# Kernel tuning notes

Measured on AMD Instinct MI355X. Metric: run time of the kernel, lower is better.

## Reference

```python
import jax, jax.numpy as jnp
import numpy as np

N_NODES = 10240
N_EDGES = 40960
N_GRAPHS = 256
F_XD = 78
SEQ = 1000
VOCAB = 26
EMB = 128
NEG_SLOPE = 0.2


def gat_conv(x, src, dst, W, att_src, att_dst, bias, heads, f_out):
    """PyG GATConv (concat=True, self-loops, leaky_relu 0.2, dst-segment softmax)."""
    N = x.shape[0]
    h = (x @ W).reshape(N, heads, f_out)                      # [N,H,F]
    a_s = jnp.sum(h * att_src[None], axis=-1)                 # [N,H]
    a_d = jnp.sum(h * att_dst[None], axis=-1)                 # [N,H]
    loop = jnp.arange(N, dtype=src.dtype)
    s = jnp.concatenate([src, loop])                          # add self-loops
    d = jnp.concatenate([dst, loop])
    e = jax.nn.leaky_relu(a_s[s] + a_d[d], NEG_SLOPE)         # [E',H]
    m = jax.ops.segment_max(e, d, num_segments=N)             # stable softmax per dst
    e = jnp.exp(e - m[d])
    denom = jax.ops.segment_sum(e, d, num_segments=N)
    alpha = e / (denom[d] + 1e-16)                            # [E',H]
    out = jax.ops.segment_sum(alpha[:, :, None] * h[s], d, num_segments=N)
    return out.reshape(N, heads * f_out) + bias


def conv1d(x, w, b):
    y = jax.lax.conv_general_dilated(x, w, window_strides=(1,), padding='VALID',
                                     dimension_numbers=('NCH', 'OIH', 'NCH'))
    return y + b[None, :, None]


def maxpool1d(x, k):
    return jax.lax.reduce_window(x, -jnp.inf, jax.lax.max, (1, 1, k), (1, 1, k), 'VALID')


def setup_inputs() -> dict:
    key = jax.random.key(0)
    ks = jax.random.split(key, 32)
    x = jax.random.normal(ks[0], (N_NODES, F_XD), jnp.float32)
    src = jax.random.randint(ks[1], (N_EDGES,), 0, N_NODES, dtype=jnp.int32)
    dst = jax.random.randint(ks[2], (N_EDGES,), 0, N_NODES, dtype=jnp.int32)
    dst = jnp.where(dst == src, (dst + 1) % N_NODES, dst)     # no pre-existing self loops
    edge_index = jnp.stack([src, dst])
    batch = jnp.repeat(jnp.arange(N_GRAPHS, dtype=jnp.int32), N_NODES // N_GRAPHS)
    target = jax.random.randint(ks[3], (N_GRAPHS, SEQ), 0, VOCAB, dtype=jnp.int32)
    def w(k, shape):
        return jax.random.normal(k, shape, jnp.float32) * 0.05
    p = {
        'W1': w(ks[4], (78, 10 * 78)), 'as1': w(ks[5], (10, 78)), 'ad1': w(ks[6], (10, 78)), 'b1': jnp.zeros((780,), jnp.float32),
        'W2': w(ks[7], (780, 2 * 780)), 'as2': w(ks[8], (2, 780)), 'ad2': w(ks[9], (2, 780)), 'b2': jnp.zeros((1560,), jnp.float32),
        'W3': w(ks[10], (1560, 3120)), 'as3': w(ks[11], (1, 3120)), 'ad3': w(ks[12], (1, 3120)), 'b3': jnp.zeros((3120,), jnp.float32),
        'fc_g1_w': w(ks[13], (3120, 1024)), 'fc_g1_b': jnp.zeros((1024,), jnp.float32),
        'fc_g2_w': w(ks[14], (1024, 128)), 'fc_g2_b': jnp.zeros((128,), jnp.float32),
        'emb_xt': w(ks[15], (VOCAB, EMB)),
        'cw1': w(ks[16], (32, 1000, 8)), 'cb1': jnp.zeros((32,), jnp.float32),
        'cw2': w(ks[17], (64, 32, 8)), 'cb2': jnp.zeros((64,), jnp.float32),
        'cw3': w(ks[18], (96, 64, 8)), 'cb3': jnp.zeros((96,), jnp.float32),
        'cw4': w(ks[19], (128, 96, 8)), 'cb4': jnp.zeros((128,), jnp.float32),
        'fc1_xt_w': w(ks[20], (128 * 33, 1024)), 'fc1_xt_b': jnp.zeros((1024,), jnp.float32),
        'fc2_xt_w': w(ks[21], (1024, 128)), 'fc2_xt_b': jnp.zeros((128,), jnp.float32),
        'fc1_w': w(ks[22], (256, 1024)), 'fc1_b': jnp.zeros((1024,), jnp.float32),
        'fc2_w': w(ks[23], (1024, 256)), 'fc2_b': jnp.zeros((256,), jnp.float32),
        'out_w': w(ks[24], (256, 1)), 'out_b': jnp.zeros((1,), jnp.float32),
    }
    return {'x': x, 'edge_index': edge_index, 'batch': batch, 'target': target, **p}


def reference(x, edge_index, batch, target,
              W1, as1, ad1, b1, W2, as2, ad2, b2, W3, as3, ad3, b3,
              fc_g1_w, fc_g1_b, fc_g2_w, fc_g2_b, emb_xt,
              cw1, cb1, cw2, cb2, cw3, cb3, cw4, cb4,
              fc1_xt_w, fc1_xt_b, fc2_xt_w, fc2_xt_b,
              fc1_w, fc1_b, fc2_w, fc2_b, out_w, out_b):
    src, dst = edge_index[0], edge_index[1]
    # --- GAT branch (dropout layers are identity in eval mode) ---
    h = jax.nn.elu(gat_conv(x, src, dst, W1, as1, ad1, b1, 10, 78))
    h = jax.nn.relu(gat_conv(h, src, dst, W2, as2, ad2, b2, 2, 780))
    h = jax.nn.relu(gat_conv(h, src, dst, W3, as3, ad3, b3, 1, 3120))
    g = jax.ops.segment_max(h, batch, num_segments=N_GRAPHS)   # global max pool
    g = jax.nn.relu(g @ fc_g1_w + fc_g1_b)
    g = g @ fc_g2_w + fc_g2_b                                  # [B,128]
    # --- protein CNN branch ---
    e = emb_xt[target]                                         # [B,1000,128]
    c = jax.nn.relu(conv1d(e, cw1, cb1))                       # [B,32,121]
    c = jax.nn.relu(conv1d(c, cw2, cb2))                       # [B,64,114]
    c = jax.nn.relu(conv1d(c, cw3, cb3))                       # [B,96,107]
    c = jax.nn.relu(conv1d(c, cw4, cb4))                       # [B,128,100]
    c = maxpool1d(c, 3)                                        # [B,128,33]
    xt = c.reshape(N_GRAPHS, 128 * 33)
    xt = jax.nn.relu(xt @ fc1_xt_w + fc1_xt_b)
    xt = xt @ fc2_xt_w + fc2_xt_b                              # [B,128]
    # --- fusion head ---
    xc = jnp.concatenate([g, xt], axis=1)                      # [B,256]
    xc = jax.nn.relu(xc @ fc1_w + fc1_b)
    xc = jax.nn.relu(xc @ fc2_w + fc2_b)
    return xc @ out_w + out_b                                  # [B,1]
```

## Files before the change

### kernel.cpp

```cpp
#include <hip/hip_runtime.h>
#include <hip/hip_bf16.h>
#include <math.h>

static const int NNODES = 10240;
static const int NEDGES = 40960;
static const int NB     = 256;
static const int VOCAB  = 26;
static const int EMB    = 128;
static const int LP     = 128;
static const int C1SPLIT = 8;

typedef short bf16x8 __attribute__((ext_vector_type(8)));
typedef float f32x4  __attribute__((ext_vector_type(4)));

__device__ __forceinline__ float bf16bits2float(short s) {
    return __uint_as_float(((unsigned)(unsigned short)s) << 16);
}

__global__ __launch_bounds__(256) void gemm_f32_splitk_sl(
    const float* __restrict__ A, const float* __restrict__ B,
    float* __restrict__ P, int M, int N, int K, int kchunk)
{
    __shared__ float As[16][65];
    __shared__ float Bs[16][65];
    int tid = threadIdx.x;
    int bm = blockIdx.y * 64;
    int bn = blockIdx.x * 64;
    int z = blockIdx.z;
    int k0 = z * kchunk;
    int k1 = min(k0 + kchunk, K);
    int tx = tid & 15, ty = tid >> 4;
    float acc[4][4] = {};
    for (int kb = k0; kb < k1; kb += 16) {
#pragma unroll
        for (int l = 0; l < 4; ++l) {
            int idx = tid + l * 256;
            int r = idx >> 4, c = idx & 15;
            int gr = bm + r, gc = kb + c;
            As[c][r] = (gr < M && gc < k1) ? A[(size_t)gr * K + gc] : 0.f;
        }
#pragma unroll
        for (int l = 0; l < 4; ++l) {
            int idx = tid + l * 256;
            int r = idx >> 6, c = idx & 63;
            int gr = kb + r, gc = bn + c;
            Bs[r][c] = (gr < k1 && gc < N) ? B[(size_t)gr * N + gc] : 0.f;
        }
        __syncthreads();
#pragma unroll
        for (int kk = 0; kk < 16; ++kk) {
            float a[4], b[4];
#pragma unroll
            for (int i = 0; i < 4; ++i) a[i] = As[kk][ty * 4 + i];
#pragma unroll
            for (int j = 0; j < 4; ++j) b[j] = Bs[kk][tx * 4 + j];
#pragma unroll
            for (int i = 0; i < 4; ++i)
#pragma unroll
                for (int j = 0; j < 4; ++j)
                    acc[i][j] += a[i] * b[j];
        }
        __syncthreads();
    }
    float* Pz = P + (size_t)z * M * N;
#pragma unroll
    for (int i = 0; i < 4; ++i) {
        int gr = bm + ty * 4 + i;
        if (gr >= M) continue;
#pragma unroll
        for (int j = 0; j < 4; ++j) {
            int gc = bn + tx * 4 + j;
            if (gc >= N) continue;
            Pz[(size_t)gr * N + gc] = acc[i][j];
        }
    }
}

template<int ACT>
__global__ void reduce_bias_act_ld_kernel(const float* __restrict__ P,
                                          const float* __restrict__ bias,
                                          float* __restrict__ C,
                                          int M, int N, int S, int ldC)
{
    int t = blockIdx.x * 256 + threadIdx.x;
    if (t >= M * N) return;
    int r = t / N, c = t - r * N;
    float v = bias[c];
    for (int s = 0; s < S; ++s) v += P[(size_t)s * M * N + t];
    if (ACT == 1) v = fmaxf(v, 0.f);
    C[(size_t)r * ldC + c] = v;
}

__global__ void out_head_kernel(const float* __restrict__ f2,
                                const float* __restrict__ w,
                                const float* __restrict__ b,
                                float* __restrict__ out)
{
    __shared__ float sw[256];
    int t = threadIdx.x;
    sw[t] = w[t];
    __syncthreads();
    float acc = 0.f;
    const float* row = f2 + (size_t)t * 256;
    for (int k = 0; k < 256; ++k) acc += row[k] * sw[k];
    out[t] = acc + b[0];
}

__global__ void cast_a_kernel(const float* __restrict__ in, __hip_bfloat16* __restrict__ out,
                              int M, int K, int Kp)
{
    int idx = blockIdx.x * 256 + threadIdx.x;
    if (idx >= M * Kp) return;
    int r = idx / Kp, k = idx - r * Kp;
    out[idx] = __float2bfloat16(k < K ? in[(size_t)r * K + k] : 0.f);
}

__global__ __launch_bounds__(256) void transpose_cast_kernel(
    const float* __restrict__ in, __hip_bfloat16* __restrict__ out,
    int K, int N, int Kp, int Npad)
{
    __shared__ float tile[32][33];
    int k0 = blockIdx.x * 32;
    int n0 = blockIdx.y * 32;
    int tx = threadIdx.x & 31;
    int ty = threadIdx.x >> 5;
#pragma unroll
    for (int j = 0; j < 4; ++j) {
        int k = k0 + ty + j * 8, n = n0 + tx;
        tile[ty + j * 8][tx] = (k < K && n < N) ? in[(size_t)k * N + n] : 0.f;
    }
    __syncthreads();
#pragma unroll
    for (int j = 0; j < 4; ++j) {
        int n = n0 + ty + j * 8, k = k0 + tx;
        if (n < Npad && k < Kp)
            out[(size_t)n * Kp + k] = __float2bfloat16(tile[tx][ty + j * 8]);
    }
}

__global__ void conv_wt_all_kernel(
    const float* __restrict__ cw2, const float* __restrict__ cw3,
    const float* __restrict__ cw4, const float* __restrict__ cw1,
    __hip_bfloat16* __restrict__ wt2, __hip_bfloat16* __restrict__ wt3,
    __hip_bfloat16* __restrict__ wt4, float* __restrict__ wt1f)
{
    int idx = blockIdx.x * 256 + threadIdx.x;
    const int n2 = 64 * 32 * 8, n3 = 96 * 64 * 8, n4 = 128 * 96 * 8;
    if (idx < n2) {
        int o = idx / (32 * 8), rem = idx - o * 32 * 8;
        int i = rem >> 3, k = rem & 7;
        wt2[(size_t)o * 256 + k * 32 + i] = __float2bfloat16(cw2[idx]);
    } else if (idx < n2 + n3) {
        int j = idx - n2;
        int o = j / (64 * 8), rem = j - o * 64 * 8;
        int i = rem >> 3, k = rem & 7;
        wt3[(size_t)o * 512 + k * 64 + i] = __float2bfloat16(cw3[j]);
    } else if (idx < n2 + n3 + n4) {
        int j = idx - n2 - n3;
        int o = j / (96 * 8), rem = j - o * 96 * 8;
        int i = rem >> 3, k = rem & 7;
        wt4[(size_t)o * 768 + k * 96 + i] = __float2bfloat16(cw4[j]);
    } else {
        int j = idx - n2 - n3 - n4;
        if (j >= 32 * 8000) return;
        int o = j / 8000, rem = j - o * 8000;
        int i = rem >> 3, k = rem & 7;
        wt1f[(size_t)i * 256 + o * 8 + k] = cw1[j];
    }
}

__device__ __forceinline__ void stage_tile(
    const __hip_bfloat16* __restrict__ gA, int ldA,
    const __hip_bfloat16* __restrict__ gB, int ldB,
    short* ldsbuf, int w, int l)
{
#pragma unroll
    for (int j = 0; j < 4; ++j) {
        int u = (w * 4 + j) * 64 + l;
        int r = u >> 3, s = u & 7;
        const __hip_bfloat16* src = gA + (size_t)r * ldA + ((s ^ (r & 7)) << 3);
        __builtin_amdgcn_global_load_lds(
            (const __attribute__((address_space(1))) void*)src,
            (__attribute__((address_space(3))) void*)(ldsbuf + (w * 4 + j) * 512),
            16, 0, 0);
    }
#pragma unroll
    for (int j = 0; j < 4; ++j) {
        int u = (w * 4 + j) * 64 + l;
        int r = u >> 3, s = u & 7;
        const __hip_bfloat16* src = gB + (size_t)r * ldB + ((s ^ (r & 7)) << 3);
        __builtin_amdgcn_global_load_lds(
            (const __attribute__((address_space(1))) void*)src,
            (__attribute__((address_space(3))) void*)(ldsbuf + 8192 + (w * 4 + j) * 512),
            16, 0, 0);
    }
}

__global__ __launch_bounds__(256, 2) void gemm_mfma_bf16(
    const __hip_bfloat16* __restrict__ A,
    const __hip_bfloat16* __restrict__ Bt,
    __hip_bfloat16* __restrict__ C, int M, int N, int Kp, int ldC)
{
    __shared__ __align__(16) short lds[2][16384];
    const int tid = threadIdx.x;
    const int w = tid >> 6, l = tid & 63;

    int nwg = gridDim.x * gridDim.y;
    int wg = blockIdx.y * gridDim.x + blockIdx.x;
    int q = nwg >> 3, r8 = nwg & 7;
    int xcd = wg & 7, lo = wg >> 3;
    int swz = (xcd < r8) ? (xcd * (q + 1) + lo) : (r8 * (q + 1) + (xcd - r8) * q + lo);
    const int bm = (swz / gridDim.x) * 128, bn = (swz % gridDim.x) * 128;

    const int wr = w >> 1, wc = w & 1;
    const int lane15 = l & 15, lhi = l >> 4;

    const __hip_bfloat16* gA = A + (size_t)bm * Kp;
    const __hip_bfloat16* gB = Bt + (size_t)bn * Kp;

    f32x4 acc[4][4] = {};

    const int nk = Kp >> 6;
    stage_tile(gA, Kp, gB, Kp, &lds[0][0], w, l);
    __syncthreads();
    int cur = 0;
    for (int t = 0; t < nk; ++t) {
        if (t + 1 < nk)
            stage_tile(gA + (t + 1) * 64, Kp, gB + (t + 1) * 64, Kp, &lds[cur ^ 1][0], w, l);
        const short* bA = &lds[cur][0];
        const short* bB = &lds[cur][8192];
#pragma unroll
        for (int ks = 0; ks < 2; ++ks) {
            bf16x8 af[4], bfr[4];
#pragma unroll
            for (int m = 0; m < 4; ++m) {
                int r = wr * 64 + m * 16 + lane15;
                int slot = (ks * 4 + lhi) ^ (r & 7);
                af[m] = *(const bf16x8*)(bA + r * 64 + slot * 8);
            }
#pragma unroll
            for (int n = 0; n < 4; ++n) {
                int r = wc * 64 + n * 16 + lane15;
                int slot = (ks * 4 + lhi) ^ (r & 7);
                bfr[n] = *(const bf16x8*)(bB + r * 64 + slot * 8);
            }
#pragma unroll
            for (int m = 0; m < 4; ++m)
#pragma unroll
                for (int n = 0; n < 4; ++n)
                    acc[m][n] = __builtin_amdgcn_mfma_f32_16x16x32_bf16(
                        af[m], bfr[n], acc[m][n], 0, 0, 0);
        }
        __syncthreads();
        cur ^= 1;
    }
#pragma unroll
    for (int m = 0; m < 4; ++m) {
#pragma unroll
        for (int n = 0; n < 4; ++n) {
            int col = bn + wc * 64 + n * 16 + lane15;
            if (col >= N) continue;
            int row0 = bm + wr * 64 + m * 16 + lhi * 4;
#pragma unroll
            for (int q2 = 0; q2 < 4; ++q2)
                C[(size_t)(row0 + q2) * ldC + col] = __float2bfloat16(acc[m][n][q2]);
        }
    }
}

__global__ __launch_bounds__(256, 2) void gemm_mfma_splitk(
    const __hip_bfloat16* __restrict__ A,
    const __hip_bfloat16* __restrict__ Bt,
    float* __restrict__ P, int M, int N, int Kp, int tps)
{
    __shared__ __align__(16) short lds[2][16384];
    const int tid = threadIdx.x;
    const int w = tid >> 6, l = tid & 63;
    const int bm = blockIdx.y * 128, bn = blockIdx.x * 128;
    const int z = blockIdx.z;
    const int wr = w >> 1, wc = w & 1;
    const int lane15 = l & 15, lhi = l >> 4;

    const __hip_bfloat16* gA = A + (size_t)bm * Kp + z * tps * 64;
    const __hip_bfloat16* gB = Bt + (size_t)bn * Kp + z * tps * 64;

    f32x4 acc[4][4] = {};

    const int nk = tps;
    stage_tile(gA, Kp, gB, Kp, &lds[0][0], w, l);
    __syncthreads();
    int cur = 0;
    for (int t = 0; t < nk; ++t) {
        if (t + 1 < nk)
            stage_tile(gA + (t + 1) * 64, Kp, gB + (t + 1) * 64, Kp, &lds[cur ^ 1][0], w, l);
        const short* bA = &lds[cur][0];
        const short* bB = &lds[cur][8192];
#pragma unroll
        for (int ks = 0; ks < 2; ++ks) {
            bf16x8 af[4], bfr[4];
#pragma unroll
            for (int m = 0; m < 4; ++m) {
                int r = wr * 64 + m * 16 + lane15;
                int slot = (ks * 4 + lhi) ^ (r & 7);
                af[m] = *(const bf16x8*)(bA + r * 64 + slot * 8);
            }
#pragma unroll
            for (int n = 0; n < 4; ++n) {
                int r = wc * 64 + n * 16 + lane15;
                int slot = (ks * 4 + lhi) ^ (r & 7);
                bfr[n] = *(const bf16x8*)(bB + r * 64 + slot * 8);
            }
#pragma unroll
            for (int m = 0; m < 4; ++m)
#pragma unroll
                for (int n = 0; n < 4; ++n)
                    acc[m][n] = __builtin_amdgcn_mfma_f32_16x16x32_bf16(
                        af[m], bfr[n], acc[m][n], 0, 0, 0);
        }
        __syncthreads();
        cur ^= 1;
    }
    float* Pz = P + (size_t)z * M * N;
#pragma unroll
    for (int m = 0; m < 4; ++m) {
#pragma unroll
        for (int n = 0; n < 4; ++n) {
            int col = bn + wc * 64 + n * 16 + lane15;
            if (col >= N) continue;
            int row0 = bm + wr * 64 + m * 16 + lhi * 4;
#pragma unroll
            for (int q2 = 0; q2 < 4; ++q2) {
                int row = row0 + q2;
                if (row < M) Pz[(size_t)row * N + col] = acc[m][n][q2];
            }
        }
    }
}

template<int Ci, int Co, int Lout>
__global__ __launch_bounds__(256, 2) void gemm_conv_bf16(
    const __hip_bfloat16* __restrict__ A,
    const __hip_bfloat16* __restrict__ Bt,
    const float* __restrict__ bias,
    __hip_bfloat16* __restrict__ C)
{
    const int Kp = 8 * Ci;
    __shared__ __align__(16) short lds[2][16384];
    const int tid = threadIdx.x;
    const int w = tid >> 6, l = tid & 63;
    const int bm = blockIdx.y * 128;
    const int wr = w >> 1, wc = w & 1;
    const int lane15 = l & 15, lhi = l >> 4;

    const __hip_bfloat16* gA = A + (size_t)bm * Ci;
    const __hip_bfloat16* gB = Bt;

    f32x4 acc[4][4] = {};

    const int nk = Kp >> 6;
    stage_tile(gA, Ci, gB, Kp, &lds[0][0], w, l);
    __syncthreads();
    int cur = 0;
    for (int t = 0; t < nk; ++t) {
        if (t + 1 < nk)
            stage_tile(gA + (t + 1) * 64, Ci, gB + (t + 1) * 64, Kp, &lds[cur ^ 1][0], w, l);
        const short* bA = &lds[cur][0];
        const short* bB = &lds[cur][8192];
#pragma unroll
        for (int ks = 0; ks < 2; ++ks) {
            bf16x8 af[4], bfr[4];
#pragma unroll
            for (int m = 0; m < 4; ++m) {
                int r = wr * 64 + m * 16 + lane15;
                int slot = (ks * 4 + lhi) ^ (r & 7);
                af[m] = *(const bf16x8*)(bA + r * 64 + slot * 8);
            }
#pragma unroll
            for (int n = 0; n < 4; ++n) {
                int r = wc * 64 + n * 16 + lane15;
                int slot = (ks * 4 + lhi) ^ (r & 7);
                bfr[n] = *(const bf16x8*)(bB + r * 64 + slot * 8);
            }
#pragma unroll
            for (int m = 0; m < 4; ++m)
#pragma unroll
                for (int n = 0; n < 4; ++n)
                    acc[m][n] = __builtin_amdgcn_mfma_f32_16x16x32_bf16(
                        af[m], bfr[n], acc[m][n], 0, 0, 0);
        }
        __syncthreads();
        cur ^= 1;
    }
#pragma unroll
    for (int m = 0; m < 4; ++m) {
#pragma unroll
        for (int n = 0; n < 4; ++n) {
            int col = wc * 64 + n * 16 + lane15;
            if (col >= Co) continue;
            float bb = bias[col];
            int lr0 = wr * 64 + m * 16 + lhi * 4;
#pragma unroll
            for (int q2 = 0; q2 < 4; ++q2) {
                int lr = lr0 + q2;
                if (lr < Lout)
                    C[((size_t)bm + lr) * Co + col] =
                        __float2bfloat16(fmaxf(acc[m][n][q2] + bb, 0.f));
            }
        }
    }
}

__global__ __launch_bounds__(256, 2) void gemm_conv4_pool_bf16(
    const __hip_bfloat16* __restrict__ A,
    const __hip_bfloat16* __restrict__ Bt,
    const float* __restrict__ bias,
    __hip_bfloat16* __restrict__ xtb)
{
    const int Ci = 96, Kp = 768;
    __shared__ __align__(16) short lds[2][16384];
    const int tid = threadIdx.x;
    const int w = tid >> 6, l = tid & 63;
    const int bm = blockIdx.y * 128;
    const int wr = w >> 1, wc = w & 1;
    const int lane15 = l & 15, lhi = l >> 4;

    const __hip_bfloat16* gA = A + (size_t)bm * Ci;
    const __hip_bfloat16* gB = Bt;

    f32x4 acc[4][4] = {};

    const int nk = Kp >> 6;
    stage_tile(gA, Ci, gB, Kp, &lds[0][0], w, l);
    __syncthreads();
    int cur = 0;
    for (int t = 0; t < nk; ++t) {
        if (t + 1 < nk)
            stage_tile(gA + (t + 1) * 64, Ci, gB + (t + 1) * 64, Kp, &lds[cur ^ 1][0], w, l);
        const short* bA = &lds[cur][0];
        const short* bB = &lds[cur][8192];
#pragma unroll
        for (int ks = 0; ks < 2; ++ks) {
            bf16x8 af[4], bfr[4];
#pragma unroll
            for (int m = 0; m < 4; ++m) {
                int r = wr * 64 + m * 16 + lane15;
                int slot = (ks * 4 + lhi) ^ (r & 7);
                af[m] = *(const bf16x8*)(bA + r * 64 + slot * 8);
            }
#pragma unroll
            for (int n = 0; n < 4; ++n) {
                int r = wc * 64 + n * 16 + lane15;
                int slot = (ks * 4 + lhi) ^ (r & 7);
                bfr[n] = *(const bf16x8*)(bB + r * 64 + slot * 8);
            }
#pragma unroll
            for (int m = 0; m < 4; ++m)
#pragma unroll
                for (int n = 0; n < 4; ++n)
                    acc[m][n] = __builtin_amdgcn_mfma_f32_16x16x32_bf16(
                        af[m], bfr[n], acc[m][n], 0, 0, 0);
        }
        __syncthreads();
        cur ^= 1;
    }
    float* pbuf = (float*)&lds[0][0];
#pragma unroll
    for (int m = 0; m < 4; ++m) {
#pragma unroll
        for (int n = 0; n < 4; ++n) {
            int col = wc * 64 + n * 16 + lane15;
            float bb = bias[col];
            int lr0 = wr * 64 + m * 16 + lhi * 4;
#pragma unroll
            for (int q2 = 0; q2 < 4; ++q2)
                pbuf[(lr0 + q2) * 128 + col] = acc[m][n][q2] + bb;
        }
    }
    __syncthreads();
    int nb = blockIdx.y;
    for (int idx = tid; idx < 4352; idx += 256) {
        __hip_bfloat16 v;
        if (idx >= 4224) {
            v = __float2bfloat16(0.f);
        } else {
            int c = idx / 33, tp = idx - c * 33;
            float m3 = fmaxf(fmaxf(pbuf[(tp * 3) * 128 + c], pbuf[(tp * 3 + 1) * 128 + c]),
                             pbuf[(tp * 3 + 2) * 128 + c]);
            v = __float2bfloat16(fmaxf(m3, 0.f));
        }
        xtb[(size_t)nb * 4352 + idx] = v;
    }
}

__global__ void attn_ab_kernel(const __hip_bfloat16* __restrict__ lin, int Ftp,
                               const float* __restrict__ att_s,
                               const float* __restrict__ att_d,
                               float* __restrict__ a_s, float* __restrict__ a_d,
                               int H, int F)
{
    int bid = blockIdx.x;
    int n = bid / H, h = bid - n * H;
    int lane = threadIdx.x;
    const __hip_bfloat16* row = lin + (size_t)n * Ftp + h * F;
    const float* wsrc = att_s + h * F;
    const float* wdst = att_d + h * F;
    float ss = 0.f, sd = 0.f;
    for (int f = lane; f < F; f += 64) {
        float v = __bfloat162float(row[f]);
        ss += v * wsrc[f];
        sd += v * wdst[f];
    }
    for (int o = 32; o; o >>= 1) {
        ss += __shfl_down(ss, o);
        sd += __shfl_down(sd, o);
    }
    if (lane == 0) { a_s[bid] = ss; a_d[bid] = sd; }
}

__global__ void deg_kernel(const int* __restrict__ ei, int* __restrict__ deg,
                           int E, int Etot)
{
    int e = blockIdx.x * 256 + threadIdx.x;
    if (e >= Etot) return;
    int d = (e < E) ? ei[E + e] : e - E;
    atomicAdd(&deg[d], 1);
}

__global__ __launch_bounds__(256) void scan_kernel(const int* __restrict__ deg,
                                                   int* __restrict__ rowptr,
                                                   int* __restrict__ cursor, int n)
{
    __shared__ int partial[256];
    int tid = threadIdx.x;
    const int per = (n + 255) / 256;
    int base = tid * per;
    int sum = 0;
    for (int i = 0; i < per; ++i) {
        int idx = base + i;
        if (idx < n) sum += deg[idx];
    }
    partial[tid] = sum;
    __syncthreads();
    for (int offs = 1; offs < 256; offs <<= 1) {
        int v = (tid >= offs) ? partial[tid - offs] : 0;
        __syncthreads();
        partial[tid] += v;
        __syncthreads();
    }
    int run = (tid == 0) ? 0 : partial[tid - 1];
    for (int i = 0; i < per; ++i) {
        int idx = base + i;
        if (idx < n) { rowptr[idx] = run; cursor[idx] = run; run += deg[idx]; }
    }
    if (tid == 255) rowptr[n] = run;
}

__global__ void fill_csr_kernel(const int* __restrict__ ei, int* __restrict__ cursor,
                                int* __restrict__ eidx, int E, int Etot)
{
    int e = blockIdx.x * 256 + threadIdx.x;
    if (e >= Etot) return;
    int d = (e < E) ? ei[E + e] : e - E;
    int pos = atomicAdd(&cursor[d], 1);
    eidx[pos] = e;
}

template<int ACT>
__global__ __launch_bounds__(64) void gat_gather8_kernel(
    const int* __restrict__ rowptr, const int* __restrict__ eidx,
    const int* __restrict__ ei,
    const float* __restrict__ a_s, const float* __restrict__ a_d,
    const __hip_bfloat16* __restrict__ lin, int Ftp,
    const float* __restrict__ bias,
    __hip_bfloat16* __restrict__ outh, int Kout,
    int E, int H, int F, int Ft)
{
    int d = blockIdx.x;
    int g = blockIdx.y * 64 + threadIdx.x;
    int c0 = g * 8;
    if (c0 >= Kout) return;
    bf16x8 res;
    if (c0 >= Ft) {
#pragma unroll
        for (int j = 0; j < 8; ++j) res[j] = 0;
        *(bf16x8*)(outh + (size_t)d * Kout + c0) = res;
        return;
    }
    int h0 = min(c0 / F, H - 1);
    int h1 = min((c0 + 7) / F, H - 1);
    int split = (h1 == h0) ? 8 : (F * (h0 + 1) - c0);
    float ad0 = a_d[d * H + h0];
    float ad1 = (h1 == h0) ? ad0 : a_d[d * H + h1];
    int p0 = rowptr[d], p1 = rowptr[d + 1];

    float m0 = -INFINITY, m1 = -INFINITY;
    for (int p = p0; p < p1; ++p) {
        int e = eidx[p];
        int s = (e < E) ? ei[e] : e - E;
        float v0 = a_s[s * H + h0] + ad0;
        v0 = v0 > 0.f ? v0 : 0.2f * v0;
        m0 = fmaxf(m0, v0);
        if (h1 != h0) {
            float v1 = a_s[s * H + h1] + ad1;
            v1 = v1 > 0.f ? v1 : 0.2f * v1;
            m1 = fmaxf(m1, v1);
        }
    }
    if (h1 == h0) m1 = m0;

    float acc[8] = {};
    float sum0 = 0.f, sum1 = 0.f;
    for (int p = p0; p < p1; ++p) {
        int e = eidx[p];
        int s = (e < E) ? ei[e] : e - E;
        float v0 = a_s[s * H + h0] + ad0;
        v0 = v0 > 0.f ? v0 : 0.2f * v0;
        float w0 = expf(v0 - m0);
        sum0 += w0;
        float w1;
        if (h1 != h0) {
            float v1 = a_s[s * H + h1] + ad1;
            v1 = v1 > 0.f ? v1 : 0.2f * v1;
            w1 = expf(v1 - m1);
            sum1 += w1;
        } else {
            w1 = w0;
        }
        bf16x8 v = *(const bf16x8*)(lin + (size_t)s * Ftp + c0);
#pragma unroll
        for (int j = 0; j < 8; ++j) {
            float wv = (j < split) ? w0 : w1;
            acc[j] += wv * bf16bits2float(v[j]);
        }
    }
    float rs0 = 1.f / (sum0 + 1e-16f);
    float rs1 = (h1 == h0) ? rs0 : 1.f / (sum1 + 1e-16f);

#pragma unroll
    for (int j = 0; j < 8; ++j) {
        int c = c0 + j;
        float val = 0.f;
        if (c < Ft) {
            val = acc[j] * ((j < split) ? rs0 : rs1) + bias[c];
            if (ACT == 1) val = fmaxf(val, 0.f);
            else if (ACT == 2) val = val > 0.f ? val : expm1f(val);
        }
        __hip_bfloat16 bv = __float2bfloat16(val);
        res[j] = *(const short*)&bv;
    }
    *(bf16x8*)(outh + (size_t)d * Kout + c0) = res;
}

__global__ void pool_max_bf16_kernel(const __hip_bfloat16* __restrict__ h,
                                     __hip_bfloat16* __restrict__ g,
                                     int B, int per, int C, int Kout)
{
    int t = blockIdx.x * blockDim.x + threadIdx.x;
    if (t >= B * Kout) return;
    int b = t / Kout, f = t - b * Kout;
    if (f >= C) { g[t] = __float2bfloat16(0.f); return; }
    const __hip_bfloat16* p = h + (size_t)b * per * C + f;
    float m = -INFINITY;
    for (int j = 0; j < per; ++j) m = fmaxf(m, __bfloat162float(p[(size_t)j * C]));
    g[t] = __float2bfloat16(m);
}

__global__ __launch_bounds__(256) void conv1_p1_kernel(
    const int* __restrict__ target, const float* __restrict__ wt,
    float* __restrict__ Spart)
{
    __shared__ float s_S[VOCAB * 256];
    __shared__ int   s_trow[125];
    int tid = threadIdx.x;
    int n = blockIdx.x, z = blockIdx.y;
    for (int i = tid; i < VOCAB * 256; i += 256) s_S[i] = 0.f;
    if (tid < 125) s_trow[tid] = target[n * 1000 + z * 125 + tid];
    __syncthreads();
    const float* wz = wt + (size_t)(z * 125) * 256 + tid;
    for (int i = 0; i < 125; ++i) {
        int v = s_trow[i];
        s_S[v * 256 + tid] += wz[(size_t)i * 256];
    }
    __syncthreads();
    float* outp = Spart + ((size_t)n * C1SPLIT + z) * (VOCAB * 256);
    for (int i = tid; i < VOCAB * 256; i += 256) outp[i] = s_S[i];
}

__global__ __launch_bounds__(256) void conv1_p2_kernel(
    const float* __restrict__ Spart, const float* __restrict__ emb,
    const float* __restrict__ b, __hip_bfloat16* __restrict__ y)
{
    __shared__ float s_emb[VOCAB * EMB];
    __shared__ float s_S[VOCAB * 256];
    int tid = threadIdx.x;
    int n = blockIdx.x;
    for (int i = tid; i < VOCAB * EMB; i += 256) s_emb[i] = emb[i];
    const float* base = Spart + (size_t)n * C1SPLIT * (VOCAB * 256);
    for (int i = tid; i < VOCAB * 256; i += 256) {
        float s = 0.f;
#pragma unroll
        for (int z = 0; z < C1SPLIT; ++z) s += base[(size_t)z * (VOCAB * 256) + i];
        s_S[i] = s;
    }
    __syncthreads();
    for (int idx = tid; idx < 121 * 32; idx += 256) {
        int t = idx >> 5, o = idx & 31;
        float acc = b[o];
#pragma unroll
        for (int v = 0; v < VOCAB; ++v) {
            const float* Sv = s_S + v * 256 + o * 8;
            const float* ev = s_emb + v * EMB + t;
#pragma unroll
            for (int k = 0; k < 8; ++k) acc += Sv[k] * ev[k];
        }
        y[((size_t)n * LP + t) * 32 + o] = __float2bfloat16(fmaxf(acc, 0.f));
    }
}

extern "C" void kernel_launch(void* const* d_in, const int* in_sizes, int n_in,
                              void* d_out, int out_size, void* d_ws, size_t ws_size,
                              hipStream_t stream)
{
    const float* x      = (const float*)d_in[0];
    const int*   ei     = (const int*)d_in[1];
    const int*   target = (const int*)d_in[3];
    const float* W1  = (const float*)d_in[4];
    const float* as1 = (const float*)d_in[5];
    const float* ad1 = (const float*)d_in[6];
    const float* b1  = (const float*)d_in[7];
    const float* W2  = (const float*)d_in[8];
    const float* as2 = (const float*)d_in[9];
    const float* ad2 = (const float*)d_in[10];
    const float* b2  = (const float*)d_in[11];
    const float* W3  = (const float*)d_in[12];
    const float* as3 = (const float*)d_in[13];
    const float* ad3 = (const float*)d_in[14];
    const float* b3  = (const float*)d_in[15];
    const float* fc_g1_w = (const float*)d_in[16];
    const float* fc_g1_b = (const float*)d_in[17];
    const float* fc_g2_w = (const float*)d_in[18];
    const float* fc_g2_b = (const float*)d_in[19];
    const float* emb_xt  = (const float*)d_in[20];
    const float* cw1 = (const float*)d_in[21];
    const float* cb1 = (const float*)d_in[22];
    const float* cw2 = (const float*)d_in[23];
    const float* cb2 = (const float*)d_in[24];
    const float* cw3 = (const float*)d_in[25];
    const float* cb3 = (const float*)d_in[26];
    const float* cw4 = (const float*)d_in[27];
    const float* cb4 = (const float*)d_in[28];
    const float* fc1_xt_w = (const float*)d_in[29];
    const float* fc1_xt_b = (const float*)d_in[30];
    const float* fc2_xt_w = (const float*)d_in[31];
    const float* fc2_xt_b = (const float*)d_in[32];
    const float* fc1_w = (const float*)d_in[33];
    const float* fc1_b = (const float*)d_in[34];
    const float* fc2_w = (const float*)d_in[35];
    const float* fc2_b = (const float*)d_in[36];
    const float* out_w = (const float*)d_in[37];
    const float* out_b = (const float*)d_in[38];
    float* out = (float*)d_out;

    const int N = NNODES, E = NEDGES, Etot = E + N;
    const size_t MB = 1024 * 1024;

    char* ws = (char*)d_ws;
    size_t off = 0;
    auto alloc = [&](size_t bytes) -> char* {
        char* p = ws + off;
        off = (off + bytes + 255) & ~(size_t)255;
        return p;
    };
    const size_t BIG = (size_t)N * 3120 * sizeof(float);
    char*  bufA  = alloc(BIG);
    char*  bufB  = alloc(BIG);
    float*    a_s   = (float*)alloc((size_t)N * 10 * 4);
    float*    a_d   = (float*)alloc((size_t)N * 10 * 4);
    float*    g1    = (float*)alloc((size_t)NB * 1024 * 4);
    float*    xt1   = (float*)alloc((size_t)NB * 1024 * 4);
    float*    xc    = (float*)alloc((size_t)NB * 256 * 4);
    float*    f1    = (float*)alloc((size_t)NB * 1024 * 4);
    float*    f2    = (float*)alloc((size_t)NB * 256 * 4);
    __hip_bfloat16* gbufb = (__hip_bfloat16*)alloc((size_t)NB * 3200 * 2);
    __hip_bfloat16* xtb   = (__hip_bfloat16*)alloc((size_t)NB * 4352 * 2);
    int*      deg     = (int*)alloc((size_t)N * 4);
    int*      rowptr  = (int*)alloc((size_t)(N + 1) * 4);
    int*      cursor  = (int*)alloc((size_t)N * 4);
    int*      eidx    = (int*)alloc((size_t)Etot * 4);

    __hip_bfloat16* linb = (__hip_bfloat16*)bufA;
    __hip_bfloat16* Wt   = (__hip_bfloat16*)(bufA + 64 * MB);
    __hip_bfloat16* xb   = (__hip_bfloat16*)(bufA + 80 * MB);
    __hip_bfloat16* hbf1 = (__hip_bfloat16*)bufB;
    __hip_bfloat16* hbf2 = (__hip_bfloat16*)(bufB + 20 * MB);
    __hip_bfloat16* hbf3 = (__hip_bfloat16*)bufB;
    __hip_bfloat16* Wt2  = (__hip_bfloat16*)(bufB + 105 * MB);
    float*          P4   = (float*)(bufB + 115 * MB);

    char* cnn = bufA;
    auto calloc2 = [&](size_t bytes) -> char* {
        char* p = cnn;
        cnn += (bytes + 255) & ~(size_t)255;
        return p;
    };
    __hip_bfloat16* act1 = (__hip_bfloat16*)calloc2((size_t)NB * LP * 32 * 2 + 4096);
    __hip_bfloat16* act2 = (__hip_bfloat16*)calloc2((size_t)NB * LP * 64 * 2 + 4096);
    __hip_bfloat16* act3 = (__hip_bfloat16*)calloc2((size_t)NB * LP * 96 * 2 + 4096);
    __hip_bfloat16* wt2  = (__hip_bfloat16*)calloc2((size_t)128 * 256 * 2);
    __hip_bfloat16* wt3  = (__hip_bfloat16*)calloc2((size_t)128 * 512 * 2);
    __hip_bfloat16* wt4  = (__hip_bfloat16*)calloc2((size_t)128 * 768 * 2);
    float* wt1f  = (float*)calloc2((size_t)1000 * 256 * 4);
    float* Spart = (float*)calloc2((size_t)NB * C1SPLIT * VOCAB * 256 * 4);

    {
        (void)hipMemsetAsync(deg, 0, (size_t)N * 4, stream);
        deg_kernel<<<(Etot + 255) / 256, 256, 0, stream>>>(ei, deg, E, Etot);
        scan_kernel<<<1, 256, 0, stream>>>(deg, rowptr, cursor, N);
        fill_csr_kernel<<<(Etot + 255) / 256, 256, 0, stream>>>(ei, cursor, eidx, E, Etot);
    }

    auto head_gemm = [&](const float* A, const float* B, const float* bias, float* C,
                         int M, int Nc, int K, int ldC, int act, int S) {
        int kchunk = (K + S - 1) / S;
        dim3 g((Nc + 63) / 64, (M + 63) / 64, S);
        gemm_f32_splitk_sl<<<g, 256, 0, stream>>>(A, B, P4, M, Nc, K, kchunk);
        int tot = M * Nc;
        if (act == 1)
            reduce_bias_act_ld_kernel<1><<<(tot + 255) / 256, 256, 0, stream>>>(P4, bias, C, M, Nc, S, ldC);
        else
            reduce_bias_act_ld_kernel<0><<<(tot + 255) / 256, 256, 0, stream>>>(P4, bias, C, M, Nc, S, ldC);
    };

    auto head_gemm_mfma = [&](const __hip_bfloat16* Ab_, const float* W, const float* bias,
                              float* C, int M, int Nc, int K, int Kp, int S) {
        int tps = (Kp / 64) / S;
        transpose_cast_kernel<<<dim3(Kp / 32, Nc / 32), 256, 0, stream>>>(W, Wt2, K, Nc, Kp, Nc);
        dim3 g(Nc / 128, M / 128, S);
        gemm_mfma_splitk<<<g, 256, 0, stream>>>(Ab_, Wt2, P4, M, Nc, Kp, tps);
        int tot = M * Nc;
        reduce_bias_act_ld_kernel<1><<<(tot + 255) / 256, 256, 0, stream>>>(P4, bias, C, M, Nc, S, Nc);
    };

    auto gat_tail = [&](const float* atts, const float* attd, const float* bias,
                        int H, int F, int Ftp, int act,
                        const __hip_bfloat16* lin, __hip_bfloat16* outh, int Kout) {
        attn_ab_kernel<<<N * H, 64, 0, stream>>>(lin, Ftp, atts, attd, a_s, a_d, H, F);
        int Ft = H * F;
        int groups = Kout / 8;
        dim3 gg(N, (groups + 63) / 64);
        if (act == 1)
            gat_gather8_kernel<1><<<gg, 64, 0, stream>>>(rowptr, eidx, ei, a_s, a_d, lin, Ftp, bias, outh, Kout, E, H, F, Ft);
        else
            gat_gather8_kernel<2><<<gg, 64, 0, stream>>>(rowptr, eidx, ei, a_s, a_d, lin, Ftp, bias, outh, Kout, E, H, F, Ft);
    };

    {
        (void)hipMemsetAsync(linb, 0, (size_t)N * 784 * 2, stream);
        cast_a_kernel<<<(N * 128 + 255) / 256, 256, 0, stream>>>(x, xb, N, 78, 128);
        transpose_cast_kernel<<<dim3(4, 28), 256, 0, stream>>>(W1, Wt, 78, 780, 128, 896);
        gemm_mfma_bf16<<<dim3(7, N / 128), 256, 0, stream>>>(xb, Wt, linb, N, 780, 128, 784);
        gat_tail(as1, ad1, b1, 10, 78, 784, 2, linb, hbf1, 832);
    }
    {
        const int Kp = 832, Nout = 1560, Npad = 1664;
        transpose_cast_kernel<<<dim3(Kp / 32, Npad / 32), 256, 0, stream>>>(W2, Wt, 780, Nout, Kp, Npad);
        gemm_mfma_bf16<<<dim3(Npad / 128, N / 128), 256, 0, stream>>>(hbf1, Wt, linb, N, Nout, Kp, Nout);
        gat_tail(as2, ad2, b2, 2, 780, 1560, 1, linb, hbf2, 1600);
    }
    {
        const int Kp = 1600, Nout = 3120, Npad = 3200;
        transpose_cast_kernel<<<dim3(Kp / 32, Npad / 32), 256, 0, stream>>>(W3, Wt, 1560, Nout, Kp, Npad);
        gemm_mfma_bf16<<<dim3(Npad / 128, N / 128), 256, 0, stream>>>(hbf2, Wt, linb, N, Nout, Kp, Nout);
        gat_tail(as3, ad3, b3, 1, 3120, 3120, 1, linb, hbf3, 3120);
    }

    {
        int tot = NB * 3200;
        pool_max_bf16_kernel<<<(tot + 255) / 256, 256, 0, stream>>>(hbf3, gbufb, NB, N / NB, 3120, 3200);
        head_gemm_mfma(gbufb, fc_g1_w, fc_g1_b, g1, NB, 1024, 3120, 3200, 5);
        head_gemm(g1, fc_g2_w, fc_g2_b, xc, NB, 128, 1024, 256, 0, 32);
    }

    {
        conv_wt_all_kernel<<<(64 * 32 * 8 + 96 * 64 * 8 + 128 * 96 * 8 + 32 * 8000 + 255) / 256,
                             256, 0, stream>>>(cw2, cw3, cw4, cw1, wt2, wt3, wt4, wt1f);
        conv1_p1_kernel<<<dim3(NB, C1SPLIT), 256, 0, stream>>>(target, wt1f, Spart);
        conv1_p2_kernel<<<NB, 256, 0, stream>>>(Spart, emb_xt, cb1, act1);
        gemm_conv_bf16<32, 64, 114><<<dim3(1, NB), 256, 0, stream>>>(act1, wt2, cb2, act2);
        gemm_conv_bf16<64, 96, 107><<<dim3(1, NB), 256, 0, stream>>>(act2, wt3, cb3, act3);
        gemm_conv4_pool_bf16<<<dim3(1, NB), 256, 0, stream>>>(act3, wt4, cb4, xtb);
        head_gemm_mfma(xtb, fc1_xt_w, fc1_xt_b, xt1, NB, 1024, 4224, 4352, 4);
        head_gemm(xt1, fc2_xt_w, fc2_xt_b, xc + 128, NB, 128, 1024, 256, 0, 32);
    }

    {
        head_gemm(xc, fc1_w, fc1_b, f1, NB, 1024, 256, 1024, 1, 8);
        head_gemm(f1, fc2_w, fc2_b, f2, NB, 256, 1024, 256, 1, 16);
        out_head_kernel<<<1, 256, 0, stream>>>(f2, out_w, out_b, out);
    }
}
```

Baseline: 759.9 us.

## Fuse the small MLP head layers into one per-row kernel

Replaces the four split-K FP32 GEMMs (fc_g2, fc2_xt, fc1, fc2), their reduce kernels and the output dot product with one kernel that processes one batch row per block. Intermediates stay in shared memory. This removes about ten launches and the partial-sum round trips through global memory. In exchange, each block re-reads the full weight matrices from global or L2 with plain per-thread loops instead of tiled reuse, so the total weight traffic grows by a factor of the batch size and relies on cache hits.

```diff
diff --git a/kernel.cpp b/kernel.cpp
--- a/kernel.cpp
+++ b/kernel.cpp
@@ -17,93 +17,72 @@
     return __uint_as_float(((unsigned)(unsigned short)s) << 16);
 }
 
-__global__ __launch_bounds__(256) void gemm_f32_splitk_sl(
-    const float* __restrict__ A, const float* __restrict__ B,
-    float* __restrict__ P, int M, int N, int K, int kchunk)
-{
-    __shared__ float As[16][65];
-    __shared__ float Bs[16][65];
-    int tid = threadIdx.x;
-    int bm = blockIdx.y * 64;
-    int bn = blockIdx.x * 64;
-    int z = blockIdx.z;
-    int k0 = z * kchunk;
-    int k1 = min(k0 + kchunk, K);
-    int tx = tid & 15, ty = tid >> 4;
-    float acc[4][4] = {};
-    for (int kb = k0; kb < k1; kb += 16) {
-#pragma unroll
-        for (int l = 0; l < 4; ++l) {
-            int idx = tid + l * 256;
-            int r = idx >> 4, c = idx & 15;
-            int gr = bm + r, gc = kb + c;
-            As[c][r] = (gr < M && gc < k1) ? A[(size_t)gr * K + gc] : 0.f;
-        }
-#pragma unroll
-        for (int l = 0; l < 4; ++l) {
-            int idx = tid + l * 256;
-            int r = idx >> 6, c = idx & 63;
-            int gr = kb + r, gc = bn + c;
-            Bs[r][c] = (gr < k1 && gc < N) ? B[(size_t)gr * N + gc] : 0.f;
-        }
-        __syncthreads();
-#pragma unroll
-        for (int kk = 0; kk < 16; ++kk) {
-            float a[4], b[4];
-#pragma unroll
-            for (int i = 0; i < 4; ++i) a[i] = As[kk][ty * 4 + i];
-#pragma unroll
-            for (int j = 0; j < 4; ++j) b[j] = Bs[kk][tx * 4 + j];
-#pragma unroll
-            for (int i = 0; i < 4; ++i)
-#pragma unroll
-                for (int j = 0; j < 4; ++j)
-                    acc[i][j] += a[i] * b[j];
-        }
-        __syncthreads();
-    }
-    float* Pz = P + (size_t)z * M * N;
-#pragma unroll
-    for (int i = 0; i < 4; ++i) {
-        int gr = bm + ty * 4 + i;
-        if (gr >= M) continue;
-#pragma unroll
-        for (int j = 0; j < 4; ++j) {
-            int gc = bn + tx * 4 + j;
-            if (gc >= N) continue;
-            Pz[(size_t)gr * N + gc] = acc[i][j];
-        }
-    }
-}
-
-template<int ACT>
-__global__ void reduce_bias_act_ld_kernel(const float* __restrict__ P,
-                                          const float* __restrict__ bias,
-                                          float* __restrict__ C,
-                                          int M, int N, int S, int ldC)
+__global__ void reduce_bias_relu_ld_kernel(const float* __restrict__ P,
+                                           const float* __restrict__ bias,
+                                           float* __restrict__ C,
+                                           int M, int N, int S, int ldC)
 {
     int t = blockIdx.x * 256 + threadIdx.x;
     if (t >= M * N) return;
     int r = t / N, c = t - r * N;
     float v = bias[c];
     for (int s = 0; s < S; ++s) v += P[(size_t)s * M * N + t];
-    if (ACT == 1) v = fmaxf(v, 0.f);
-    C[(size_t)r * ldC + c] = v;
-}
-
-__global__ void out_head_kernel(const float* __restrict__ f2,
-                                const float* __restrict__ w,
-                                const float* __restrict__ b,
-                                float* __restrict__ out)
-{
-    __shared__ float sw[256];
-    int t = threadIdx.x;
-    sw[t] = w[t];
-    __syncthreads();
-    float acc = 0.f;
-    const float* row = f2 + (size_t)t * 256;
-    for (int k = 0; k < 256; ++k) acc += row[k] * sw[k];
-    out[t] = acc + b[0];
+    C[(size_t)r * ldC + c] = fmaxf(v, 0.f);
+}
+
+__global__ __launch_bounds__(256) void fused_head_kernel(
+    const float* __restrict__ g1, const float* __restrict__ xt1,
+    const float* __restrict__ fc_g2_w, const float* __restrict__ fc_g2_b,
+    const float* __restrict__ fc2_xt_w, const float* __restrict__ fc2_xt_b,
+    const float* __restrict__ fc1_w, const float* __restrict__ fc1_b,
+    const float* __restrict__ fc2_w, const float* __restrict__ fc2_b,
+    const float* __restrict__ out_w, const float* __restrict__ out_b,
+    float* __restrict__ out)
+{
+    __shared__ float s_in[2048];
+    __shared__ float s_xc[256];
+    __shared__ float s_f1[1024];
+    __shared__ float s_f2[256];
+    __shared__ float s_part[4];
+    int r = blockIdx.x, t = threadIdx.x;
+    for (int i = t; i < 1024; i += 256) {
+        s_in[i]        = g1[(size_t)r * 1024 + i];
+        s_in[1024 + i] = xt1[(size_t)r * 1024 + i];
+    }
+    __syncthreads();
+    {
+        const float* W  = (t < 128) ? fc_g2_w : fc2_xt_w;
+        const float* bb = (t < 128) ? fc_g2_b : fc2_xt_b;
+        const float* in = (t < 128) ? s_in : s_in + 1024;
+        int c = t & 127;
+        float acc = bb[c];
+        for (int k = 0; k < 1024; ++k)
+            acc += in[k] * W[k * 128 + c];
+        s_xc[t] = acc;
+    }
+    __syncthreads();
+#pragma unroll
+    for (int jj = 0; jj < 4; ++jj) {
+        int j = t + jj * 256;
+        float acc = fc1_b[j];
+        for (int k = 0; k < 256; ++k)
+            acc += s_xc[k] * fc1_w[k * 1024 + j];
+        s_f1[j] = fmaxf(acc, 0.f);
+    }
+    __syncthreads();
+    {
+        float acc = fc2_b[t];
+        for (int k = 0; k < 1024; ++k)
+            acc += s_f1[k] * fc2_w[k * 256 + t];
+        s_f2[t] = fmaxf(acc, 0.f);
+    }
+    __syncthreads();
+    float p = s_f2[t] * out_w[t];
+    for (int o = 32; o; o >>= 1) p += __shfl_down(p, o);
+    if ((t & 63) == 0) s_part[t >> 6] = p;
+    __syncthreads();
+    if (t == 0)
+        out[r] = s_part[0] + s_part[1] + s_part[2] + s_part[3] + out_b[0];
 }
 
 __global__ void cast_a_kernel(const float* __restrict__ in, __hip_bfloat16* __restrict__ out,
@@ -778,9 +757,6 @@
     float*    a_d   = (float*)alloc((size_t)N * 10 * 4);
     float*    g1    = (float*)alloc((size_t)NB * 1024 * 4);
     float*    xt1   = (float*)alloc((size_t)NB * 1024 * 4);
-    float*    xc    = (float*)alloc((size_t)NB * 256 * 4);
-    float*    f1    = (float*)alloc((size_t)NB * 1024 * 4);
-    float*    f2    = (float*)alloc((size_t)NB * 256 * 4);
     __hip_bfloat16* gbufb = (__hip_bfloat16*)alloc((size_t)NB * 3200 * 2);
     __hip_bfloat16* xtb   = (__hip_bfloat16*)alloc((size_t)NB * 4352 * 2);
     int*      deg     = (int*)alloc((size_t)N * 4);
@@ -819,18 +795,6 @@
         fill_csr_kernel<<<(Etot + 255) / 256, 256, 0, stream>>>(ei, cursor, eidx, E, Etot);
     }
 
-    auto head_gemm = [&](const float* A, const float* B, const float* bias, float* C,
-                         int M, int Nc, int K, int ldC, int act, int S) {
-        int kchunk = (K + S - 1) / S;
-        dim3 g((Nc + 63) / 64, (M + 63) / 64, S);
-        gemm_f32_splitk_sl<<<g, 256, 0, stream>>>(A, B, P4, M, Nc, K, kchunk);
-        int tot = M * Nc;
-        if (act == 1)
-            reduce_bias_act_ld_kernel<1><<<(tot + 255) / 256, 256, 0, stream>>>(P4, bias, C, M, Nc, S, ldC);
-        else
-            reduce_bias_act_ld_kernel<0><<<(tot + 255) / 256, 256, 0, stream>>>(P4, bias, C, M, Nc, S, ldC);
-    };
-
     auto head_gemm_mfma = [&](const __hip_bfloat16* Ab_, const float* W, const float* bias,
                               float* C, int M, int Nc, int K, int Kp, int S) {
         int tps = (Kp / 64) / S;
@@ -838,7 +802,7 @@
         dim3 g(Nc / 128, M / 128, S);
         gemm_mfma_splitk<<<g, 256, 0, stream>>>(Ab_, Wt2, P4, M, Nc, Kp, tps);
         int tot = M * Nc;
-        reduce_bias_act_ld_kernel<1><<<(tot + 255) / 256, 256, 0, stream>>>(P4, bias, C, M, Nc, S, Nc);
+        reduce_bias_relu_ld_kernel<<<(tot + 255) / 256, 256, 0, stream>>>(P4, bias, C, M, Nc, S, Nc);
     };
 
     auto gat_tail = [&](const float* atts, const float* attd, const float* bias,
@@ -878,7 +842,6 @@
         int tot = NB * 3200;
         pool_max_bf16_kernel<<<(tot + 255) / 256, 256, 0, stream>>>(hbf3, gbufb, NB, N / NB, 3120, 3200);
         head_gemm_mfma(gbufb, fc_g1_w, fc_g1_b, g1, NB, 1024, 3120, 3200, 5);
-        head_gemm(g1, fc_g2_w, fc_g2_b, xc, NB, 128, 1024, 256, 0, 32);
     }
 
     {
@@ -890,12 +853,9 @@
         gemm_conv_bf16<64, 96, 107><<<dim3(1, NB), 256, 0, stream>>>(act2, wt3, cb3, act3);
         gemm_conv4_pool_bf16<<<dim3(1, NB), 256, 0, stream>>>(act3, wt4, cb4, xtb);
         head_gemm_mfma(xtb, fc1_xt_w, fc1_xt_b, xt1, NB, 1024, 4224, 4352, 4);
-        head_gemm(xt1, fc2_xt_w, fc2_xt_b, xc + 128, NB, 128, 1024, 256, 0, 32);
-    }
-
-    {
-        head_gemm(xc, fc1_w, fc1_b, f1, NB, 1024, 256, 1024, 1, 8);
-        head_gemm(f1, fc2_w, fc2_b, f2, NB, 256, 1024, 256, 1, 16);
-        out_head_kernel<<<1, 256, 0, stream>>>(f2, out_w, out_b, out);
-    }
-}
+    }
+
+    fused_head_kernel<<<NB, 256, 0, stream>>>(
+        g1, xt1, fc_g2_w, fc_g2_b, fc2_xt_w, fc2_xt_b,
+        fc1_w, fc1_b, fc2_w, fc2_b, out_w, out_b, out);
+}
```

After: 758.5 us. About the same (-0.2%).
